# Kernel optimization log

Hardware: AMD Instinct MI355X
Metric: run time of the kernel (lower is better)

## Reference

```python
import jax, jax.numpy as jnp
import numpy as np

EMBED_DIM = 1024
NUM_HEADS = 16
HEAD_DIM = EMBED_DIM // NUM_HEADS


def setup_inputs() -> dict:
    key = jax.random.key(0)
    k_x, k_qw, k_qb, k_ow, k_ob = jax.random.split(key, 5)
    B, T, C = 2, 2048, EMBED_DIM
    scale = 1.0 / np.sqrt(C)
    return {
        "x": jax.random.normal(k_x, (B, T, C), dtype=jnp.float32),
        "qkv_w": jax.random.normal(k_qw, (C, 3 * C), dtype=jnp.float32) * scale,
        "qkv_b": jax.random.normal(k_qb, (3 * C,), dtype=jnp.float32) * 0.02,
        "out_w": jax.random.normal(k_ow, (C, C), dtype=jnp.float32) * scale,
        "out_b": jax.random.normal(k_ob, (C,), dtype=jnp.float32) * 0.02,
    }


def reference(x, qkv_w, qkv_b, out_w, out_b):
    # x: (B, T, C). Causal masked multi-head self-attention (eval mode: dropout off).
    B, T, C = x.shape
    H, Dh = NUM_HEADS, HEAD_DIM
    qkv = x @ qkv_w + qkv_b                      # (B, T, 3C)
    qkv = qkv.reshape(B, T, 3, H, Dh)
    q = jnp.transpose(qkv[:, :, 0], (0, 2, 1, 3))  # (B, H, T, Dh)
    k = jnp.transpose(qkv[:, :, 1], (0, 2, 1, 3))
    v = jnp.transpose(qkv[:, :, 2], (0, 2, 1, 3))
    scores = jnp.einsum("bhqd,bhkd->bhqk", q, k) / np.sqrt(Dh)
    causal = jnp.tril(jnp.ones((T, T), dtype=bool))
    scores = jnp.where(causal[None, None], scores, -jnp.inf)
    attn = jax.nn.softmax(scores, axis=-1)        # (B, H, T, T)
    out = jnp.einsum("bhqk,bhkd->bhqd", attn, v)  # (B, H, T, Dh)
    out = jnp.transpose(out, (0, 2, 1, 3)).reshape(B, T, C)
    return out @ out_w + out_b
```

## Files before the change

kernel.cpp:

```cpp
#include <hip/hip_runtime.h>


typedef __bf16 bf16;
typedef __attribute__((ext_vector_type(4))) __bf16 bf16x4;
typedef __attribute__((ext_vector_type(8))) __bf16 bf16x8;
typedef __attribute__((ext_vector_type(4))) float f32x4;

#define T_SEQ 2048
#define NHEAD 16
#define QSCALE 0.1803368801111244f

__device__ __forceinline__ void async16(const bf16* g, const bf16* l) {
    __builtin_amdgcn_global_load_lds(
        (const __attribute__((address_space(1))) void*)g,
        (__attribute__((address_space(3))) void*)l, 16, 0, 0);
}

__global__ __launch_bounds__(256) void prep(
    const float* __restrict__ x, bf16* __restrict__ xb,
    const float* __restrict__ qkv_w, bf16* __restrict__ wbT,
    const float* __restrict__ out_w, bf16* __restrict__ owbT) {
    const int bid = blockIdx.x, tid = threadIdx.x;
    if (bid < 4096) {
        int i = (bid * 256 + tid) * 4;
        float4 v = *(const float4*)(x + i);
        bf16x4 o;
        o.x = (bf16)v.x; o.y = (bf16)v.y; o.z = (bf16)v.z; o.w = (bf16)v.w;
        *(bf16x4*)(xb + i) = o;
        return;
    }
    __shared__ float tile[32][33];
    const float* in;
    bf16* out;
    int K_, N_, b;
    if (bid < 7168) { b = bid - 4096; in = qkv_w; out = wbT; K_ = 1024; N_ = 3072; }
    else            { b = bid - 7168; in = out_w; out = owbT; K_ = 1024; N_ = 1024; }
    int k0 = (b & 31) * 32, n0 = (b >> 5) * 32;
    int tx = tid & 31, ty = tid >> 5;
    for (int r = 0; r < 32; r += 8)
        tile[ty + r][tx] = in[(k0 + ty + r) * N_ + n0 + tx];
    __syncthreads();
    for (int r = 0; r < 32; r += 8)
        out[(n0 + ty + r) * K_ + k0 + tx] = (bf16)tile[tx][ty + r];
}

__global__ __launch_bounds__(256) void gemm_qkv(
    const bf16* __restrict__ A, const bf16* __restrict__ Bt,
    const float* __restrict__ bias,
    bf16* __restrict__ Qo, bf16* __restrict__ Ko, bf16* __restrict__ Vt) {
    __shared__ __align__(16) bf16 As[128 * 32];
    __shared__ __align__(16) bf16 Bs[128 * 32];
    const int t = threadIdx.x;
    const int lane = t & 63, wave = t >> 6;
    const int l15 = lane & 15, quad = lane >> 4;
    const int wm = wave & 1, wn = wave >> 1;
    const int m0 = blockIdx.y * 128, n0 = blockIdx.x * 128;
    const int sec = n0 >> 10;

    f32x4 acc[4][4] = {};

    const int sfat = t >> 3, sp = t & 7;
    const int slg = sp ^ (sfat & 7);
    const int smrow = sfat * 2 + (slg >> 2);
    const int skoff = (slg & 3) << 3;
    const bf16* ag = A + (m0 + smrow) * 1024 + skoff;
    const bf16* bg = Bt + (n0 + smrow) * 1024 + skoff;
    bf16* as0 = As + wave * 512;
    bf16* as1 = As + 2048 + wave * 512;
    bf16* bs0 = Bs + wave * 512;
    bf16* bs1 = Bs + 2048 + wave * 512;

    const int foff = (l15 >> 1) * 64 + (((((l15 & 1) << 2) | quad)) ^ (l15 >> 1)) * 8;

    if (sec < 2) {
        for (int k0 = 0; k0 < 1024; k0 += 32) {
            async16(ag + k0, as0);
            async16(ag + 64 * 1024 + k0, as1);
            async16(bg + k0, bs0);
            async16(bg + 64 * 1024 + k0, bs1);
            __syncthreads();
            bf16x8 af[4], bfr[4];
            for (int i = 0; i < 4; i++)
                af[i] = *(const bf16x8*)(As + (wm * 64 + i * 16) * 32 + foff);
            for (int j = 0; j < 4; j++)
                bfr[j] = *(const bf16x8*)(Bs + (wn * 64 + j * 16) * 32 + foff);
            for (int j = 0; j < 4; j++)
                for (int i = 0; i < 4; i++)
                    acc[j][i] = __builtin_amdgcn_mfma_f32_16x16x32_bf16(bfr[j], af[i], acc[j][i], 0, 0, 0);
            __syncthreads();
        }
        bf16* dst = (sec == 0) ? Qo : Ko;
        const float sc = (sec == 0) ? QSCALE : 1.0f;
        for (int j = 0; j < 4; j++) {
            int col0 = n0 + wn * 64 + j * 16 + quad * 4;
            float4 bv = *(const float4*)(bias + col0);
            int c2 = col0 & 1023, h = c2 >> 6, d0 = c2 & 63;
            for (int i = 0; i < 4; i++) {
                int row = m0 + wm * 64 + i * 16 + l15;
                int b = row >> 11, tt = row & 2047;
                int bh = b * NHEAD + h;
                bf16x4 o;
                o[0] = (bf16)((acc[j][i][0] + bv.x) * sc);
                o[1] = (bf16)((acc[j][i][1] + bv.y) * sc);
                o[2] = (bf16)((acc[j][i][2] + bv.z) * sc);
                o[3] = (bf16)((acc[j][i][3] + bv.w) * sc);
                *(bf16x4*)(dst + (bh * T_SEQ + tt) * 64 + d0) = o;
            }
        }
    } else {
        for (int k0 = 0; k0 < 1024; k0 += 32) {
            async16(ag + k0, as0);
            async16(ag + 64 * 1024 + k0, as1);
            async16(bg + k0, bs0);
            async16(bg + 64 * 1024 + k0, bs1);
            __syncthreads();
            bf16x8 af[4], bfr[4];
            for (int i = 0; i < 4; i++)
                af[i] = *(const bf16x8*)(As + (wm * 64 + i * 16) * 32 + foff);
            for (int j = 0; j < 4; j++)
                bfr[j] = *(const bf16x8*)(Bs + (wn * 64 + j * 16) * 32 + foff);
            for (int i = 0; i < 4; i++)
                for (int j = 0; j < 4; j++)
                    acc[i][j] = __builtin_amdgcn_mfma_f32_16x16x32_bf16(af[i], bfr[j], acc[i][j], 0, 0, 0);
            __syncthreads();
        }
        for (int j = 0; j < 4; j++) {
            int col = n0 + wn * 64 + j * 16 + l15;
            float bv = bias[col];
            int c2 = col & 1023, h = c2 >> 6, d = c2 & 63;
            for (int i = 0; i < 4; i++) {
                int row0 = m0 + wm * 64 + i * 16 + quad * 4;
                int b = row0 >> 11, tt0 = row0 & 2047;
                int bh = b * NHEAD + h;
                bf16x4 o;
                for (int r = 0; r < 4; r++)
                    o[r] = (bf16)(acc[i][j][r] + bv);
                *(bf16x4*)(Vt + (bh * 64 + d) * T_SEQ + tt0) = o;
            }
        }
    }
}

#define PST 80
__global__ __launch_bounds__(256, 4) void attn(
    const bf16* __restrict__ Q, const bf16* __restrict__ K,
    const bf16* __restrict__ Vt, bf16* __restrict__ AO) {
    __shared__ __align__(16) bf16 Ks[2][64 * 64];
    __shared__ __align__(16) bf16 Vs[2][64 * 64];
    __shared__ __align__(16) bf16 Pa[4][16 * PST];
    const int tid = threadIdx.x;
    const int lane = tid & 63, wave = tid >> 6;
    const int l15 = lane & 15, quad = lane >> 4;
    const int xcdr = blockIdx.x & 7;
    const int i_ = blockIdx.x >> 3;
    const int bh = (xcdr << 2) | (i_ & 3);
    const int ti = i_ >> 2;
    const int qt = (ti & 1) ? (ti >> 1) : (31 - (ti >> 1));
    const int t0w = qt * 64 + wave * 16;

    const bf16* kp = K + bh * T_SEQ * 64;
    const bf16* vp = Vt + bh * 64 * T_SEQ;
    bf16* pw = &Pa[wave][0];
    const int b_ = bh >> 4, h_ = bh & 15;

    const int sx = (quad ^ (l15 & 7)) << 3;

    const bf16* qp = Q + (bh * T_SEQ + t0w) * 64;
    bf16x8 qf0 = *(const bf16x8*)(qp + l15 * 64 + quad * 8);
    bf16x8 qf1 = *(const bf16x8*)(qp + l15 * 64 + 32 + quad * 8);

    auto stage = [&](int kb, int b) {
        for (int i = 0; i < 2; i++) {
            int row = i * 32 + (tid >> 3), p = tid & 7;
            const bf16* ksrc = kp + (kb + row) * 64 + ((p ^ (row & 7)) << 3);
            async16(ksrc, &Ks[b][i * 2048 + wave * 512]);
            const bf16* vsrc = vp + row * T_SEQ + kb + ((p ^ (row & 7)) << 3);
            async16(vsrc, &Vs[b][i * 2048 + wave * 512]);
        }
    };

    f32x4 acc[4] = {};
    float lsum = 0.0f;

    const int C = qt + 1;
    stage(0, 0);
    for (int c = 0; c < C; c++) {
        __syncthreads();
        if (c + 1 < C) stage((c + 1) * 64, (c + 1) & 1);
        const bf16* ksb = &Ks[c & 1][0];
        const bf16* vsb = &Vs[c & 1][0];
        const bool dg = (c == qt);
        const int na = dg ? (wave + 1) : 4;

        f32x4 sc[4];
        for (int n = 0; n < 4; n++) {
            if (n < na) {
                const bf16* kbase = ksb + (n * 16 + l15) * 64;
                bf16x8 kf0 = *(const bf16x8*)(kbase + sx);
                bf16x8 kf1 = *(const bf16x8*)(kbase + (sx ^ 32));
                f32x4 z = {};
                z = __builtin_amdgcn_mfma_f32_16x16x32_bf16(kf0, qf0, z, 0, 0, 0);
                z = __builtin_amdgcn_mfma_f32_16x16x32_bf16(kf1, qf1, z, 0, 0, 0);
                sc[n] = z;
            }
        }
        for (int n = 0; n < 4; n++) {
            bf16x4 pv;
            if (n < na) {
                const bool dmask = dg && (n == na - 1);
                for (int r = 0; r < 4; r++) {
                    float v = sc[n][r];
                    if (dmask && (quad * 4 + r > l15)) v = -100000.0f;
                    float e = __builtin_amdgcn_exp2f(v);
                    lsum += e;
                    pv[r] = (bf16)e;
                }
            } else {
                pv[0] = pv[1] = pv[2] = pv[3] = (bf16)0.0f;
            }
            *(bf16x4*)(pw + l15 * PST + n * 16 + quad * 4) = pv;
        }
        __builtin_amdgcn_s_waitcnt(0xC07F);
        for (int g = 0; g < 2; g++) {
            bf16x8 pf = *(const bf16x8*)(pw + l15 * PST + g * 32 + quad * 8);
            for (int j = 0; j < 4; j++) {
                const bf16* vbase = vsb + (j * 16 + l15) * 64;
                bf16x8 vf = *(const bf16x8*)(vbase + (g ? (sx ^ 32) : sx));
                acc[j] = __builtin_amdgcn_mfma_f32_16x16x32_bf16(pf, vf, acc[j], 0, 0, 0);
            }
        }
    }

    lsum += __shfl_xor(lsum, 16);
    lsum += __shfl_xor(lsum, 32);
    float linv = 1.0f / lsum;

    bf16* aop = AO + (b_ * T_SEQ + t0w) * 1024 + h_ * 64;
    for (int r = 0; r < 4; r++) {
        float lr = __shfl(linv, quad * 4 + r, 16);
        for (int j = 0; j < 4; j++)
            aop[(quad * 4 + r) * 1024 + j * 16 + l15] = (bf16)(acc[j][r] * lr);
    }
}

__global__ __launch_bounds__(256) void gemm_out_k(
    const bf16* __restrict__ A, const bf16* __restrict__ Bt,
    const float* __restrict__ bias, float* __restrict__ out) {
    __shared__ __align__(16) bf16 As[64 * 32];
    __shared__ __align__(16) bf16 Bs[128 * 32];
    const int t = threadIdx.x;
    const int lane = t & 63, wave = t >> 6;
    const int l15 = lane & 15, quad = lane >> 4;
    const int wm = wave & 1, wn = wave >> 1;
    const int m0 = blockIdx.y * 64, n0 = blockIdx.x * 128;

    f32x4 acc[4][2] = {};

    const int sfat = t >> 3, sp = t & 7;
    const int slg = sp ^ (sfat & 7);
    const int smrow = sfat * 2 + (slg >> 2);
    const int skoff = (slg & 3) << 3;
    const bf16* ag = A + (m0 + smrow) * 1024 + skoff;
    const bf16* bg = Bt + (n0 + smrow) * 1024 + skoff;
    bf16* as0 = As + wave * 512;
    bf16* bs0 = Bs + wave * 512;
    bf16* bs1 = Bs + 2048 + wave * 512;

    const int foff = (l15 >> 1) * 64 + (((((l15 & 1) << 2) | quad)) ^ (l15 >> 1)) * 8;

    for (int k0 = 0; k0 < 1024; k0 += 32) {
        async16(ag + k0, as0);
        async16(bg + k0, bs0);
        async16(bg + 64 * 1024 + k0, bs1);
        __syncthreads();
        bf16x8 af[2], bfr[4];
        for (int i = 0; i < 2; i++)
            af[i] = *(const bf16x8*)(As + (wm * 32 + i * 16) * 32 + foff);
        for (int j = 0; j < 4; j++)
            bfr[j] = *(const bf16x8*)(Bs + (wn * 64 + j * 16) * 32 + foff);
        for (int j = 0; j < 4; j++)
            for (int i = 0; i < 2; i++)
                acc[j][i] = __builtin_amdgcn_mfma_f32_16x16x32_bf16(bfr[j], af[i], acc[j][i], 0, 0, 0);
        __syncthreads();
    }

    for (int j = 0; j < 4; j++) {
        int col0 = n0 + wn * 64 + j * 16 + quad * 4;
        float4 bv = *(const float4*)(bias + col0);
        for (int i = 0; i < 2; i++) {
            int row = m0 + wm * 32 + i * 16 + l15;
            float4 o;
            o.x = acc[j][i][0] + bv.x;
            o.y = acc[j][i][1] + bv.y;
            o.z = acc[j][i][2] + bv.z;
            o.w = acc[j][i][3] + bv.w;
            *(float4*)(out + row * 1024 + col0) = o;
        }
    }
}

extern "C" void kernel_launch(void* const* d_in, const int* in_sizes, int n_in,
                              void* d_out, int out_size, void* d_ws, size_t ws_size,
                              hipStream_t stream) {
    const float* x     = (const float*)d_in[0];
    const float* qkv_w = (const float*)d_in[1];
    const float* qkv_b = (const float*)d_in[2];
    const float* out_w = (const float*)d_in[3];
    const float* out_b = (const float*)d_in[4];
    float* out = (float*)d_out;

    char* ws = (char*)d_ws;
    bf16* xb   = (bf16*)(ws);
    bf16* wbT  = (bf16*)(ws + (8ull << 20));
    bf16* owbT = (bf16*)(ws + (14ull << 20));
    bf16* Qb   = (bf16*)(ws + (16ull << 20));
    bf16* Kb   = (bf16*)(ws + (24ull << 20));
    bf16* Vt   = (bf16*)(ws + (32ull << 20));
    bf16* AO   = (bf16*)(ws + (40ull << 20));

    prep<<<8192, 256, 0, stream>>>(x, xb, qkv_w, wbT, out_w, owbT);
    gemm_qkv<<<dim3(24, 32), 256, 0, stream>>>(xb, wbT, qkv_b, Qb, Kb, Vt);
    attn<<<1024, 256, 0, stream>>>(Qb, Kb, Vt, AO);
    gemm_out_k<<<dim3(8, 64), 256, 0, stream>>>(AO, owbT, out_b, out);
}
```

Baseline: 174.6 us.

## Use 128-row query tiles with 8 waves per attention block

Each attention workgroup now has 512 threads (8 waves) and covers 128 query rows instead of 64. Each staged K/V tile is shared by twice as many waves, which halves K/V global-to-LDS traffic per query. Staging is reorganized so each thread issues one async load per tile, and waves whose rows lie entirely before a key tile skip compute while still hitting the barrier. The tradeoffs are idle waves on diagonal tiles, half as many workgroups, and a new qt schedule that pairs short and long tiles for load balance.

```diff
diff --git a/kernel.cpp b/kernel.cpp
--- a/kernel.cpp
+++ b/kernel.cpp
@@ -142,21 +142,20 @@
 }
 
 #define PST 80
-__global__ __launch_bounds__(256, 4) void attn(
+__global__ __launch_bounds__(512, 4) void attn(
     const bf16* __restrict__ Q, const bf16* __restrict__ K,
     const bf16* __restrict__ Vt, bf16* __restrict__ AO) {
     __shared__ __align__(16) bf16 Ks[2][64 * 64];
     __shared__ __align__(16) bf16 Vs[2][64 * 64];
-    __shared__ __align__(16) bf16 Pa[4][16 * PST];
+    __shared__ __align__(16) bf16 Pa[8][16 * PST];
     const int tid = threadIdx.x;
     const int lane = tid & 63, wave = tid >> 6;
     const int l15 = lane & 15, quad = lane >> 4;
-    const int xcdr = blockIdx.x & 7;
-    const int i_ = blockIdx.x >> 3;
-    const int bh = (xcdr << 2) | (i_ & 3);
-    const int ti = i_ >> 2;
-    const int qt = (ti & 1) ? (ti >> 1) : (31 - (ti >> 1));
-    const int t0w = qt * 64 + wave * 16;
+    const int bh = ((blockIdx.x & 7) << 2) | ((blockIdx.x >> 3) & 3);
+    const int s = blockIdx.x >> 5;
+    const int qt = (s < 8) ? s : (23 - s);
+    const int t0w = qt * 128 + wave * 16;
+    const int m = t0w >> 4;
 
     const bf16* kp = K + bh * T_SEQ * 64;
     const bf16* vp = Vt + bh * 64 * T_SEQ;
@@ -170,63 +169,64 @@
     bf16x8 qf1 = *(const bf16x8*)(qp + l15 * 64 + 32 + quad * 8);
 
     auto stage = [&](int kb, int b) {
-        for (int i = 0; i < 2; i++) {
-            int row = i * 32 + (tid >> 3), p = tid & 7;
-            const bf16* ksrc = kp + (kb + row) * 64 + ((p ^ (row & 7)) << 3);
-            async16(ksrc, &Ks[b][i * 2048 + wave * 512]);
-            const bf16* vsrc = vp + row * T_SEQ + kb + ((p ^ (row & 7)) << 3);
-            async16(vsrc, &Vs[b][i * 2048 + wave * 512]);
-        }
+        int rowi = tid >> 3, p = tid & 7;
+        const bf16* ksrc = kp + (kb + rowi) * 64 + ((p ^ (rowi & 7)) << 3);
+        async16(ksrc, &Ks[b][wave * 512]);
+        const bf16* vsrc = vp + rowi * T_SEQ + kb + ((p ^ (rowi & 7)) << 3);
+        async16(vsrc, &Vs[b][wave * 512]);
     };
 
     f32x4 acc[4] = {};
     float lsum = 0.0f;
 
-    const int C = qt + 1;
+    const int C = 2 * qt + 2;
     stage(0, 0);
     for (int c = 0; c < C; c++) {
         __syncthreads();
         if (c + 1 < C) stage((c + 1) * 64, (c + 1) & 1);
-        const bf16* ksb = &Ks[c & 1][0];
-        const bf16* vsb = &Vs[c & 1][0];
-        const bool dg = (c == qt);
-        const int na = dg ? (wave + 1) : 4;
-
-        f32x4 sc[4];
-        for (int n = 0; n < 4; n++) {
-            if (n < na) {
-                const bf16* kbase = ksb + (n * 16 + l15) * 64;
-                bf16x8 kf0 = *(const bf16x8*)(kbase + sx);
-                bf16x8 kf1 = *(const bf16x8*)(kbase + (sx ^ 32));
-                f32x4 z = {};
-                z = __builtin_amdgcn_mfma_f32_16x16x32_bf16(kf0, qf0, z, 0, 0, 0);
-                z = __builtin_amdgcn_mfma_f32_16x16x32_bf16(kf1, qf1, z, 0, 0, 0);
-                sc[n] = z;
-            }
-        }
-        for (int n = 0; n < 4; n++) {
-            bf16x4 pv;
-            if (n < na) {
-                const bool dmask = dg && (n == na - 1);
-                for (int r = 0; r < 4; r++) {
-                    float v = sc[n][r];
-                    if (dmask && (quad * 4 + r > l15)) v = -100000.0f;
-                    float e = __builtin_amdgcn_exp2f(v);
-                    lsum += e;
-                    pv[r] = (bf16)e;
+        const int nr = m - 4 * c + 1;
+        if (nr > 0) {
+            const int na = min(4, nr);
+            const bool dgc = (nr <= 4);
+            const bf16* ksb = &Ks[c & 1][0];
+            const bf16* vsb = &Vs[c & 1][0];
+
+            f32x4 sc[4];
+            for (int n = 0; n < 4; n++) {
+                if (n < na) {
+                    const bf16* kbase = ksb + (n * 16 + l15) * 64;
+                    bf16x8 kf0 = *(const bf16x8*)(kbase + sx);
+                    bf16x8 kf1 = *(const bf16x8*)(kbase + (sx ^ 32));
+                    f32x4 z = {};
+                    z = __builtin_amdgcn_mfma_f32_16x16x32_bf16(kf0, qf0, z, 0, 0, 0);
+                    z = __builtin_amdgcn_mfma_f32_16x16x32_bf16(kf1, qf1, z, 0, 0, 0);
+                    sc[n] = z;
                 }
-            } else {
-                pv[0] = pv[1] = pv[2] = pv[3] = (bf16)0.0f;
-            }
-            *(bf16x4*)(pw + l15 * PST + n * 16 + quad * 4) = pv;
-        }
-        __builtin_amdgcn_s_waitcnt(0xC07F);
-        for (int g = 0; g < 2; g++) {
-            bf16x8 pf = *(const bf16x8*)(pw + l15 * PST + g * 32 + quad * 8);
-            for (int j = 0; j < 4; j++) {
-                const bf16* vbase = vsb + (j * 16 + l15) * 64;
-                bf16x8 vf = *(const bf16x8*)(vbase + (g ? (sx ^ 32) : sx));
-                acc[j] = __builtin_amdgcn_mfma_f32_16x16x32_bf16(pf, vf, acc[j], 0, 0, 0);
+            }
+            for (int n = 0; n < 4; n++) {
+                bf16x4 pv;
+                if (n < na) {
+                    const bool dmask = dgc && (n == na - 1);
+                    for (int r = 0; r < 4; r++) {
+                        float v = sc[n][r];
+                        if (dmask && (quad * 4 + r > l15)) v = -100000.0f;
+                        float e = __builtin_amdgcn_exp2f(v);
+                        lsum += e;
+                        pv[r] = (bf16)e;
+                    }
+                } else {
+                    pv[0] = pv[1] = pv[2] = pv[3] = (bf16)0.0f;
+                }
+                *(bf16x4*)(pw + l15 * PST + n * 16 + quad * 4) = pv;
+            }
+            __builtin_amdgcn_s_waitcnt(0xC07F);
+            for (int g = 0; g < 2; g++) {
+                bf16x8 pf = *(const bf16x8*)(pw + l15 * PST + g * 32 + quad * 8);
+                for (int j = 0; j < 4; j++) {
+                    const bf16* vbase = vsb + (j * 16 + l15) * 64;
+                    bf16x8 vf = *(const bf16x8*)(vbase + (g ? (sx ^ 32) : sx));
+                    acc[j] = __builtin_amdgcn_mfma_f32_16x16x32_bf16(pf, vf, acc[j], 0, 0, 0);
+                }
             }
         }
     }
@@ -320,6 +320,6 @@
 
     prep<<<8192, 256, 0, stream>>>(x, xb, qkv_w, wbT, out_w, owbT);
     gemm_qkv<<<dim3(24, 32), 256, 0, stream>>>(xb, wbT, qkv_b, Qb, Kb, Vt);
-    attn<<<1024, 256, 0, stream>>>(Qb, Kb, Vt, AO);
+    attn<<<512, 512, 0, stream>>>(Qb, Kb, Vt, AO);
     gemm_out_k<<<dim3(8, 64), 256, 0, stream>>>(AO, owbT, out_b, out);
 }
```

Result: slower. 181.4 us (+3.9%).
